# Kernel optimization log

Measured on AMD Instinct MI355X. Metric: run time of the kernel, lower is better.

Reference implementation:

```python
import math
import jax, jax.numpy as jnp
import numpy as np

BS, Q_LEN, DIM = 8, 16, 4096
MAX_SEQ = 4096
N_Q_HEADS, N_KV_HEADS, HEAD_DIM = 32, 8, 128
REP = N_Q_HEADS // N_KV_HEADS


def setup_inputs() -> dict:
    key = jax.random.key(0)
    ks = jax.random.split(key, 12)
    w = 0.02
    return {
        "x": jax.random.normal(ks[0], (BS, Q_LEN, DIM), jnp.float32),
        "k_cache": jax.random.normal(ks[1], (BS, MAX_SEQ, N_KV_HEADS, HEAD_DIM), jnp.float32),
        "v_cache": jax.random.normal(ks[2], (BS, MAX_SEQ, N_KV_HEADS, HEAD_DIM), jnp.float32),
        "Wq": jax.random.normal(ks[3], (DIM, N_Q_HEADS * HEAD_DIM), jnp.float32) * w,
        "bq": jax.random.normal(ks[4], (N_Q_HEADS * HEAD_DIM,), jnp.float32) * w,
        "Wk": jax.random.normal(ks[5], (DIM, N_KV_HEADS * HEAD_DIM), jnp.float32) * w,
        "bk": jax.random.normal(ks[6], (N_KV_HEADS * HEAD_DIM,), jnp.float32) * w,
        "Wv": jax.random.normal(ks[7], (DIM, N_KV_HEADS * HEAD_DIM), jnp.float32) * w,
        "bv": jax.random.normal(ks[8], (N_KV_HEADS * HEAD_DIM,), jnp.float32) * w,
        "Wo": jax.random.normal(ks[9], (N_Q_HEADS * HEAD_DIM, DIM), jnp.float32) * w,
        "bo": jax.random.normal(ks[10], (DIM,), jnp.float32) * w,
        "start_pos": MAX_SEQ - Q_LEN,
        "seq_len_for_kv": Q_LEN,
    }


def reference(x, k_cache, v_cache, Wq, bq, Wk, bk, Wv, bv, Wo, bo, start_pos, seq_len_for_kv):
    bs, sl, dim = x.shape
    # Projections (torch Linear: x @ W^T + b; here W stored as [in, out])
    q = (x @ Wq + bq).reshape(bs, sl, N_KV_HEADS, REP, HEAD_DIM)  # [b, q, g, r, d]
    k = (x @ Wk + bk).reshape(bs, sl, N_KV_HEADS, HEAD_DIM)
    v = (x @ Wv + bv).reshape(bs, sl, N_KV_HEADS, HEAD_DIM)
    # KV-cache append (start_pos / seq_len_for_kv are static Python ints)
    k_cache = k_cache.at[:, start_pos:start_pos + seq_len_for_kv].set(k)
    v_cache = v_cache.at[:, start_pos:start_pos + seq_len_for_kv].set(v)
    kv_len = start_pos + seq_len_for_kv
    keys = k_cache[:, :kv_len]    # [b, L, g, d]
    vals = v_cache[:, :kv_len]    # [b, L, g, d]
    # GQA: each kv head g serves REP query heads r (broadcast instead of repeat_kv)
    scale = 1.0 / math.sqrt(HEAD_DIM)
    scores = jnp.einsum('bqgrd,blgd->bgrql', q, keys) * scale  # [b, g, r, q, L]
    att = jax.nn.softmax(scores, axis=-1)
    out = jnp.einsum('bgrql,blgd->bqgrd', att, vals)           # [b, q, g, r, d]
    out = out.reshape(bs, sl, N_Q_HEADS * HEAD_DIM)
    return out @ Wo + bo
```

## Files before the change

kernel.cpp:

```cpp
#include <hip/hip_runtime.h>
#include <math.h>

#define DIM       4096
#define NKVH      8
#define HD        128
#define MAX_SEQ   4096
#define START_POS 4080
#define NQKV      6144
#define NCHUNK    8
#define CHUNK     512
#define KS        8
#define ATT_SCALE 0.08838834764831845f

#define WS_PART   0
#define WS_QH     6291456
#define WS_QL     6553600
#define WS_KNEW   6815744
#define WS_VNEW   6946816
#define WS_PM     7077888
#define WS_PL     7110656
#define WS_ATH    7143424
#define WS_ATL    7405568
#define WS_XH     7667712
#define WS_XL     7929856
#define WS_PARTO  WS_PART

typedef __bf16 bf16x8 __attribute__((ext_vector_type(8)));
typedef float  f32x4  __attribute__((ext_vector_type(4)));
typedef unsigned int uintx4 __attribute__((ext_vector_type(4)));

__device__ __forceinline__ unsigned short f2bf(float f) {
    return __builtin_bit_cast(unsigned short, (__bf16)f);
}
__device__ __forceinline__ float bf2f(unsigned short h) {
    union { unsigned int u; float f; } v; v.u = ((unsigned int)h) << 16;
    return v.f;
}
__device__ __forceinline__ void splitbf(float f, unsigned short &h, unsigned short &l) {
    h = f2bf(f);
    l = f2bf(f - bf2f(h));
}
__device__ __forceinline__ bf16x8 ldsfrag(const unsigned short* p) {
    uintx4 u = *(const uintx4*)p;
    return __builtin_bit_cast(bf16x8, u);
}
__device__ __forceinline__ bf16x8 ldsfrag2(const unsigned short* p) {
    union { uint2 u2[2]; bf16x8 v; } u;
    u.u2[0] = *(const uint2*)p;
    u.u2[1] = *(const uint2*)(p + 4);
    return u.v;
}
#define MFMA16(a,b,c) __builtin_amdgcn_mfma_f32_16x16x32_bf16(a, b, c, 0, 0, 0)
#define VCOMP(v,j) ((j)==0?(v).x:((j)==1?(v).y:((j)==2?(v).z:(v).w)))

__global__ __launch_bounds__(256) void split_x_kernel(
    const float* __restrict__ x, unsigned short* __restrict__ xh,
    unsigned short* __restrict__ xl, int n)
{
    int i = blockIdx.x * 256 + threadIdx.x;
    if (i < n) { unsigned short h, l; splitbf(x[i], h, l); xh[i] = h; xl[i] = l; }
}

__device__ __forceinline__ void gemm_body(
    const unsigned short* __restrict__ Ah, const unsigned short* __restrict__ Al,
    const float* __restrict__ W, int ldW, int noff,
    float* __restrict__ part, int partStride, int ncol0, int ks,
    unsigned short* Ahs, unsigned short* Als, unsigned short* Bs)
{
    const int t = threadIdx.x;
    const int w = t >> 6, lane = t & 63, l15 = lane & 15, quad = lane >> 4;
    f32x4 acc[2][4];
    #pragma unroll
    for (int i = 0; i < 2; ++i)
        #pragma unroll
        for (int nt = 0; nt < 4; ++nt) acc[i][nt] = (f32x4){0.f, 0.f, 0.f, 0.f};

    const int k0base = ks * 512;
    uintx4 areg_h[4], areg_l[4];
    float4 wreg[4];

    auto LOAD = [&](int it) {
        int k0 = k0base + it * 64;
        #pragma unroll
        for (int i = 0; i < 4; ++i) {
            int f = t + i * 256;
            int row = f >> 3, c0 = (f & 7) << 3;
            size_t off = (size_t)row * DIM + k0 + c0;
            areg_h[i] = *(const uintx4*)(Ah + off);
            areg_l[i] = *(const uintx4*)(Al + off);
        }
        #pragma unroll
        for (int i = 0; i < 4; ++i) {
            int kk = (t >> 4) + 16 * i;
            int n0 = (t & 15) << 2;
            wreg[i] = *(const float4*)(W + (size_t)(k0 + kk) * ldW + noff + n0);
        }
    };

    LOAD(0);
    for (int it = 0; it < 8; ++it) {
        __syncthreads();
        #pragma unroll
        for (int i = 0; i < 4; ++i) {
            int f = t + i * 256;
            int row = f >> 3, c0 = (f & 7) << 3;
            *(uintx4*)(Ahs + row * 72 + c0) = areg_h[i];
            *(uintx4*)(Als + row * 72 + c0) = areg_l[i];
        }
        {
            int n0 = (t & 15) << 2;
            #pragma unroll
            for (int i = 0; i < 4; ++i) {
                int kk = (t >> 4) + 16 * i;
                #pragma unroll
                for (int j = 0; j < 4; ++j)
                    Bs[(n0 + j) * 68 + kk] = f2bf(VCOMP(wreg[i], j));
            }
        }
        __syncthreads();
        if (it < 7) LOAD(it + 1);
        #pragma unroll
        for (int kt = 0; kt < 2; ++kt) {
            int ko = kt * 32 + quad * 8;
            bf16x8 ah0 = ldsfrag(Ahs + ((2*w+0)*16 + l15) * 72 + ko);
            bf16x8 ah1 = ldsfrag(Ahs + ((2*w+1)*16 + l15) * 72 + ko);
            bf16x8 al0 = ldsfrag(Als + ((2*w+0)*16 + l15) * 72 + ko);
            bf16x8 al1 = ldsfrag(Als + ((2*w+1)*16 + l15) * 72 + ko);
            #pragma unroll
            for (int nt = 0; nt < 4; ++nt) {
                bf16x8 b = ldsfrag2(Bs + (nt*16 + l15) * 68 + ko);
                acc[0][nt] = MFMA16(ah0, b, acc[0][nt]);
                acc[0][nt] = MFMA16(al0, b, acc[0][nt]);
                acc[1][nt] = MFMA16(ah1, b, acc[1][nt]);
                acc[1][nt] = MFMA16(al1, b, acc[1][nt]);
            }
        }
    }
    #pragma unroll
    for (int i = 0; i < 2; ++i)
        #pragma unroll
        for (int nt = 0; nt < 4; ++nt)
            #pragma unroll
            for (int r = 0; r < 4; ++r) {
                int row = (2*w + i) * 16 + quad * 4 + r;
                int col = ncol0 + nt * 16 + l15;
                part[(size_t)(ks * 128 + row) * partStride + col] = acc[i][nt][r];
            }
}

__global__ __launch_bounds__(256) void qkv_gemm_kernel(
    const unsigned short* __restrict__ xh, const unsigned short* __restrict__ xl,
    const float* __restrict__ Wq, const float* __restrict__ Wk,
    const float* __restrict__ Wv, float* __restrict__ part)
{
    __shared__ unsigned short Ahs[128 * 72], Als[128 * 72];
    __shared__ unsigned short Bs[64 * 68];
    int ncol0 = blockIdx.x * 64;
    int ks = blockIdx.y;
    const float* W; int ldW, noff;
    if (ncol0 < 4096)      { W = Wq; ldW = 4096; noff = ncol0; }
    else if (ncol0 < 5120) { W = Wk; ldW = 1024; noff = ncol0 - 4096; }
    else                   { W = Wv; ldW = 1024; noff = ncol0 - 5120; }
    gemm_body(xh, xl, W, ldW, noff, part, NQKV, ncol0, ks, Ahs, Als, Bs);
}

__global__ __launch_bounds__(256) void oproj_gemm_kernel(
    const unsigned short* __restrict__ ah, const unsigned short* __restrict__ al,
    const float* __restrict__ Wo, float* __restrict__ part)
{
    __shared__ unsigned short Ahs[128 * 72], Als[128 * 72];
    __shared__ unsigned short Bs[64 * 68];
    int ncol0 = blockIdx.x * 64;
    int ks = blockIdx.y;
    gemm_body(ah, al, Wo, 4096, ncol0, part, 4096, ncol0, ks, Ahs, Als, Bs);
}

__global__ __launch_bounds__(256) void qkv_reduce_kernel(
    const float* __restrict__ part, const float* __restrict__ bq,
    const float* __restrict__ bk, const float* __restrict__ bv,
    unsigned short* __restrict__ qh, unsigned short* __restrict__ ql,
    float* __restrict__ k_new, float* __restrict__ v_new)
{
    int gid = blockIdx.x * 256 + threadIdx.x;
    int row = gid / NQKV;
    int n   = gid - row * NQKV;
    float s = 0.f;
    #pragma unroll
    for (int j = 0; j < KS; ++j)
        s += part[(size_t)(j * 128 + row) * NQKV + n];
    if (n < 4096) {
        float v = s + bq[n];
        unsigned short h, l; splitbf(v, h, l);
        qh[row * 4096 + n] = h; ql[row * 4096 + n] = l;
    } else if (n < 5120) k_new[row * 1024 + (n - 4096)] = s + bk[n - 4096];
    else                 v_new[row * 1024 + (n - 5120)] = s + bv[n - 5120];
}

__global__ __launch_bounds__(512, 2) void attn_partial5_kernel(
    const unsigned short* __restrict__ qhp, const unsigned short* __restrict__ qlp,
    const float* __restrict__ kc, const float* __restrict__ vc,
    const float* __restrict__ knew, const float* __restrict__ vnew,
    float* __restrict__ part_O, float* __restrict__ part_m, float* __restrict__ part_l)
{
    __shared__ unsigned short Kb[2][32][136];
    __shared__ unsigned short Vt[2][128][44];
    __shared__ unsigned short Pw[8][16 * 36];

    const int t = threadIdx.x;
    const int w = t >> 6, lane = t & 63, l15 = lane & 15, quad = lane >> 4;
    const int gsel = w >> 2;
    const int rep  = w & 3;
    const int blk = blockIdx.x;
    const int b = blk >> 5, gg = (blk >> 3) & 3, c = blk & 7;
    const int g = gg * 2 + gsel;

    const int p0 = t >> 6;
    const int q4 = t & 63;
    const int gl = q4 >> 5;
    const int d0 = (q4 & 31) << 2;

    bf16x8 qhf[4], qlf[4];
    {
        size_t base = (size_t)(b * 16 + l15) * DIM + (g * 4 + rep) * HD + quad * 8;
        #pragma unroll
        for (int kt = 0; kt < 4; ++kt) {
            qhf[kt] = ldsfrag(qhp + base + kt * 32);
            qlf[kt] = ldsfrag(qlp + base + kt * 32);
        }
    }

    float m_run[4], l_run[4];
    f32x4 oacc[8];
    #pragma unroll
    for (int r = 0; r < 4; ++r) { m_run[r] = -INFINITY; l_run[r] = 0.f; }
    #pragma unroll
    for (int d = 0; d < 8; ++d) oacc[d] = (f32x4){0.f, 0.f, 0.f, 0.f};

    float4 kreg[4], vreg[4];
    auto LOADKV = [&](int it) {
        #pragma unroll
        for (int i = 0; i < 4; ++i) {
            int pos = p0 + i * 8;
            int pg = c * CHUNK + it * 32 + pos;
            const float *ksrc, *vsrc;
            if (pg >= START_POS) {
                size_t off = (size_t)(b * 16 + pg - START_POS) * (NKVH * HD) + gg * 256 + q4 * 4;
                ksrc = knew + off; vsrc = vnew + off;
            } else {
                size_t off = ((size_t)(b * MAX_SEQ + pg) * NKVH) * HD + gg * 256 + q4 * 4;
                ksrc = kc + off; vsrc = vc + off;
            }
            kreg[i] = *(const float4*)ksrc;
            vreg[i] = *(const float4*)vsrc;
        }
    };

    unsigned short* phw = Pw[w];

    LOADKV(0);
    for (int it = 0; it < 16; ++it) {
        __syncthreads();
        #pragma unroll
        for (int i = 0; i < 4; ++i) {
            int pos = p0 + i * 8;
            ushort4 k4 = make_ushort4(f2bf(kreg[i].x), f2bf(kreg[i].y),
                                      f2bf(kreg[i].z), f2bf(kreg[i].w));
            *(ushort4*)&Kb[gl][pos][d0] = k4;
        }
        #pragma unroll
        for (int j = 0; j < 4; ++j) {
            ushort4 v4 = make_ushort4(f2bf(VCOMP(vreg[0], j)), f2bf(VCOMP(vreg[1], j)),
                                      f2bf(VCOMP(vreg[2], j)), f2bf(VCOMP(vreg[3], j)));
            *(ushort4*)&Vt[gl][d0 + j][p0 * 4] = v4;
        }
        __syncthreads();
        if (it + 1 < 16) LOADKV(it + 1);

        f32x4 sacc[2];
        sacc[0] = (f32x4){0.f,0.f,0.f,0.f};
        sacc[1] = (f32x4){0.f,0.f,0.f,0.f};
        #pragma unroll
        for (int nt = 0; nt < 2; ++nt)
            #pragma unroll
            for (int kt = 0; kt < 4; ++kt) {
                bf16x8 bh = ldsfrag(&Kb[gsel][nt*16 + l15][kt*32 + quad*8]);
                sacc[nt] = MFMA16(qhf[kt], bh, sacc[nt]);
                sacc[nt] = MFMA16(qlf[kt], bh, sacc[nt]);
            }

        float e0[4], e1[4], alpha[4];
        #pragma unroll
        for (int r = 0; r < 4; ++r) {
            float s0 = sacc[0][r] * ATT_SCALE;
            float s1 = sacc[1][r] * ATT_SCALE;
            float mx = fmaxf(s0, s1);
            mx = fmaxf(mx, __shfl_xor(mx, 1));
            mx = fmaxf(mx, __shfl_xor(mx, 2));
            mx = fmaxf(mx, __shfl_xor(mx, 4));
            mx = fmaxf(mx, __shfl_xor(mx, 8));
            float mnew = fmaxf(m_run[r], mx);
            alpha[r] = __expf(m_run[r] - mnew);
            e0[r] = __expf(s0 - mnew);
            e1[r] = __expf(s1 - mnew);
            float sum = e0[r] + e1[r];
            sum += __shfl_xor(sum, 1);
            sum += __shfl_xor(sum, 2);
            sum += __shfl_xor(sum, 4);
            sum += __shfl_xor(sum, 8);
            l_run[r] = l_run[r] * alpha[r] + sum;
            m_run[r] = mnew;
        }
        #pragma unroll
        for (int d = 0; d < 8; ++d)
            #pragma unroll
            for (int r = 0; r < 4; ++r) oacc[d][r] *= alpha[r];

        {
            int slot0 = 4 * (l15 & 7) + (l15 >> 3);
            #pragma unroll
            for (int r = 0; r < 4; ++r) {
                phw[(quad*4 + r) * 36 + slot0]     = f2bf(e0[r]);
                phw[(quad*4 + r) * 36 + slot0 + 2] = f2bf(e1[r]);
            }
        }
        bf16x8 pa = ldsfrag(phw + l15 * 36 + quad * 8);

        #pragma unroll
        for (int dt = 0; dt < 8; ++dt) {
            bf16x8 vb = ldsfrag(&Vt[gsel][dt*16 + l15][quad * 8]);
            oacc[dt] = MFMA16(pa, vb, oacc[dt]);
        }
    }

    const size_t obase = (size_t)((b * 8 + g) * 8 + c) * 64 + rep * 16 + quad * 4;
    #pragma unroll
    for (int dt = 0; dt < 8; ++dt)
        #pragma unroll
        for (int r = 0; r < 4; ++r)
            part_O[(obase + r) * HD + dt * 16 + l15] = oacc[dt][r];
    if (l15 == 0) {
        #pragma unroll
        for (int r = 0; r < 4; ++r) {
            part_m[obase + r] = m_run[r];
            part_l[obase + r] = l_run[r];
        }
    }
}

__global__ __launch_bounds__(128) void attn_combine_kernel(
    const float* __restrict__ part_O, const float* __restrict__ part_m,
    const float* __restrict__ part_l, unsigned short* __restrict__ ah,
    unsigned short* __restrict__ al)
{
    int bid = blockIdx.x;
    int d = threadIdx.x;
    int bg = bid >> 6;
    int row = bid & 63;
    float mc[NCHUNK], lc[NCHUNK];
    float M = -INFINITY;
    #pragma unroll
    for (int cc = 0; cc < NCHUNK; ++cc) {
        mc[cc] = part_m[(bg * NCHUNK + cc) * 64 + row];
        lc[cc] = part_l[(bg * NCHUNK + cc) * 64 + row];
        M = fmaxf(M, mc[cc]);
    }
    float L = 0.f, acc = 0.f;
    #pragma unroll
    for (int cc = 0; cc < NCHUNK; ++cc) {
        float wgt = __expf(mc[cc] - M);
        L += lc[cc] * wgt;
        acc += part_O[((size_t)(bg * NCHUNK + cc) * 64 + row) * HD + d] * wgt;
    }
    int b = bg >> 3, g = bg & 7;
    int r = row >> 4, qp = row & 15;
    float v = acc / L;
    unsigned short h, l; splitbf(v, h, l);
    size_t idx = (size_t)(b * 16 + qp) * DIM + (g * 4 + r) * HD + d;
    ah[idx] = h; al[idx] = l;
}

__global__ __launch_bounds__(256) void oproj_reduce_kernel(
    const float* __restrict__ part, const float* __restrict__ bo,
    float* __restrict__ out)
{
    int gid = blockIdx.x * 256 + threadIdx.x;
    int n = gid & 4095;
    float s = 0.f;
    #pragma unroll
    for (int j = 0; j < KS; ++j) s += part[(size_t)j * 524288 + gid];
    out[gid] = s + bo[n];
}

extern "C" void kernel_launch(void* const* d_in, const int* in_sizes, int n_in,
                              void* d_out, int out_size, void* d_ws, size_t ws_size,
                              hipStream_t stream)
{
    const float* x  = (const float*)d_in[0];
    const float* kc = (const float*)d_in[1];
    const float* vc = (const float*)d_in[2];
    const float* Wq = (const float*)d_in[3];
    const float* bq = (const float*)d_in[4];
    const float* Wk = (const float*)d_in[5];
    const float* bk = (const float*)d_in[6];
    const float* Wv = (const float*)d_in[7];
    const float* bv = (const float*)d_in[8];
    const float* Wo = (const float*)d_in[9];
    const float* bo = (const float*)d_in[10];
    float* out = (float*)d_out;
    float* ws  = (float*)d_ws;

    unsigned short* xh = (unsigned short*)(ws + WS_XH);
    unsigned short* xl = (unsigned short*)(ws + WS_XL);
    unsigned short* qh = (unsigned short*)(ws + WS_QH);
    unsigned short* ql = (unsigned short*)(ws + WS_QL);
    unsigned short* ath = (unsigned short*)(ws + WS_ATH);
    unsigned short* atl = (unsigned short*)(ws + WS_ATL);

    split_x_kernel<<<2048, 256, 0, stream>>>(x, xh, xl, 524288);
    qkv_gemm_kernel<<<dim3(96, KS), 256, 0, stream>>>(xh, xl, Wq, Wk, Wv, ws + WS_PART);
    qkv_reduce_kernel<<<3072, 256, 0, stream>>>(ws + WS_PART, bq, bk, bv,
                                                qh, ql, ws + WS_KNEW, ws + WS_VNEW);
    attn_partial5_kernel<<<256, 512, 0, stream>>>(qh, ql, kc, vc,
                                                  ws + WS_KNEW, ws + WS_VNEW,
                                                  ws + WS_PARTO, ws + WS_PM, ws + WS_PL);
    attn_combine_kernel<<<4096, 128, 0, stream>>>(ws + WS_PARTO, ws + WS_PM,
                                                  ws + WS_PL, ath, atl);
    oproj_gemm_kernel<<<dim3(64, KS), 256, 0, stream>>>(ath, atl, Wo, ws + WS_PART);
    oproj_reduce_kernel<<<2048, 256, 0, stream>>>(ws + WS_PART, bo, out);
}
```

Before: 438.9 us.

## Double attention KV tile to 64 positions and vectorize split/reduce kernels

The attention kernel now processes 64 KV positions per iteration instead of 32, halving loop trips and barriers and issuing twice as many MFMAs and loads per sync. The P and V tiles are widened to match, with a new slot layout. The split and reduce kernels are vectorized to float4 loads and stores with a quarter of the threads. In exchange, the larger register prefetch (16 float4) and bigger LDS footprint may strain occupancy under the 512x2 launch bound.

```diff
diff --git a/kernel.cpp b/kernel.cpp
--- a/kernel.cpp
+++ b/kernel.cpp
@@ -55,10 +55,19 @@
 
 __global__ __launch_bounds__(256) void split_x_kernel(
     const float* __restrict__ x, unsigned short* __restrict__ xh,
-    unsigned short* __restrict__ xl, int n)
+    unsigned short* __restrict__ xl, int n4)
 {
     int i = blockIdx.x * 256 + threadIdx.x;
-    if (i < n) { unsigned short h, l; splitbf(x[i], h, l); xh[i] = h; xl[i] = l; }
+    if (i < n4) {
+        float4 v = *(const float4*)(x + (size_t)i * 4);
+        ushort4 h, l;
+        splitbf(v.x, h.x, l.x);
+        splitbf(v.y, h.y, l.y);
+        splitbf(v.z, h.z, l.z);
+        splitbf(v.w, h.w, l.w);
+        *(ushort4*)(xh + (size_t)i * 4) = h;
+        *(ushort4*)(xl + (size_t)i * 4) = l;
+    }
 }
 
 __device__ __forceinline__ void gemm_body(
@@ -182,29 +191,44 @@
     float* __restrict__ k_new, float* __restrict__ v_new)
 {
     int gid = blockIdx.x * 256 + threadIdx.x;
-    int row = gid / NQKV;
-    int n   = gid - row * NQKV;
-    float s = 0.f;
-    #pragma unroll
-    for (int j = 0; j < KS; ++j)
-        s += part[(size_t)(j * 128 + row) * NQKV + n];
+    int row = gid / 1536;
+    int c4  = gid - row * 1536;
+    int n = c4 * 4;
+    float4 s = make_float4(0.f, 0.f, 0.f, 0.f);
+    #pragma unroll
+    for (int j = 0; j < KS; ++j) {
+        float4 p = *(const float4*)&part[(size_t)(j * 128 + row) * NQKV + n];
+        s.x += p.x; s.y += p.y; s.z += p.z; s.w += p.w;
+    }
     if (n < 4096) {
-        float v = s + bq[n];
-        unsigned short h, l; splitbf(v, h, l);
-        qh[row * 4096 + n] = h; ql[row * 4096 + n] = l;
-    } else if (n < 5120) k_new[row * 1024 + (n - 4096)] = s + bk[n - 4096];
-    else                 v_new[row * 1024 + (n - 5120)] = s + bv[n - 5120];
-}
-
-__global__ __launch_bounds__(512, 2) void attn_partial5_kernel(
+        float4 b4 = *(const float4*)&bq[n];
+        ushort4 h, l;
+        splitbf(s.x + b4.x, h.x, l.x);
+        splitbf(s.y + b4.y, h.y, l.y);
+        splitbf(s.z + b4.z, h.z, l.z);
+        splitbf(s.w + b4.w, h.w, l.w);
+        *(ushort4*)&qh[row * 4096 + n] = h;
+        *(ushort4*)&ql[row * 4096 + n] = l;
+    } else if (n < 5120) {
+        float4 b4 = *(const float4*)&bk[n - 4096];
+        float4 o = make_float4(s.x + b4.x, s.y + b4.y, s.z + b4.z, s.w + b4.w);
+        *(float4*)&k_new[row * 1024 + (n - 4096)] = o;
+    } else {
+        float4 b4 = *(const float4*)&bv[n - 5120];
+        float4 o = make_float4(s.x + b4.x, s.y + b4.y, s.z + b4.z, s.w + b4.w);
+        *(float4*)&v_new[row * 1024 + (n - 5120)] = o;
+    }
+}
+
+__global__ __launch_bounds__(512, 2) void attn_partial7_kernel(
     const unsigned short* __restrict__ qhp, const unsigned short* __restrict__ qlp,
     const float* __restrict__ kc, const float* __restrict__ vc,
     const float* __restrict__ knew, const float* __restrict__ vnew,
     float* __restrict__ part_O, float* __restrict__ part_m, float* __restrict__ part_l)
 {
-    __shared__ unsigned short Kb[2][32][136];
-    __shared__ unsigned short Vt[2][128][44];
-    __shared__ unsigned short Pw[8][16 * 36];
+    __shared__ unsigned short Kb[2][64][136];
+    __shared__ unsigned short Vt[2][128][76];
+    __shared__ unsigned short Pw[8][16 * 76];
 
     const int t = threadIdx.x;
     const int w = t >> 6, lane = t & 63, l15 = lane & 15, quad = lane >> 4;
@@ -236,12 +260,12 @@
     #pragma unroll
     for (int d = 0; d < 8; ++d) oacc[d] = (f32x4){0.f, 0.f, 0.f, 0.f};
 
-    float4 kreg[4], vreg[4];
+    float4 kreg[8], vreg[8];
     auto LOADKV = [&](int it) {
         #pragma unroll
-        for (int i = 0; i < 4; ++i) {
+        for (int i = 0; i < 8; ++i) {
             int pos = p0 + i * 8;
-            int pg = c * CHUNK + it * 32 + pos;
+            int pg = c * CHUNK + it * 64 + pos;
             const float *ksrc, *vsrc;
             if (pg >= START_POS) {
                 size_t off = (size_t)(b * 16 + pg - START_POS) * (NKVH * HD) + gg * 256 + q4 * 4;
@@ -256,12 +280,13 @@
     };
 
     unsigned short* phw = Pw[w];
+    const int slotbase = (l15 & 7) * 8 + (l15 >> 3);
 
     LOADKV(0);
-    for (int it = 0; it < 16; ++it) {
+    for (int it = 0; it < 8; ++it) {
         __syncthreads();
         #pragma unroll
-        for (int i = 0; i < 4; ++i) {
+        for (int i = 0; i < 8; ++i) {
             int pos = p0 + i * 8;
             ushort4 k4 = make_ushort4(f2bf(kreg[i].x), f2bf(kreg[i].y),
                                       f2bf(kreg[i].z), f2bf(kreg[i].w));
@@ -269,18 +294,21 @@
         }
         #pragma unroll
         for (int j = 0; j < 4; ++j) {
-            ushort4 v4 = make_ushort4(f2bf(VCOMP(vreg[0], j)), f2bf(VCOMP(vreg[1], j)),
-                                      f2bf(VCOMP(vreg[2], j)), f2bf(VCOMP(vreg[3], j)));
-            *(ushort4*)&Vt[gl][d0 + j][p0 * 4] = v4;
+            ushort4 vlo = make_ushort4(f2bf(VCOMP(vreg[0], j)), f2bf(VCOMP(vreg[1], j)),
+                                       f2bf(VCOMP(vreg[2], j)), f2bf(VCOMP(vreg[3], j)));
+            ushort4 vhi = make_ushort4(f2bf(VCOMP(vreg[4], j)), f2bf(VCOMP(vreg[5], j)),
+                                       f2bf(VCOMP(vreg[6], j)), f2bf(VCOMP(vreg[7], j)));
+            *(ushort4*)&Vt[gl][d0 + j][p0 * 8]     = vlo;
+            *(ushort4*)&Vt[gl][d0 + j][p0 * 8 + 4] = vhi;
         }
         __syncthreads();
-        if (it + 1 < 16) LOADKV(it + 1);
-
-        f32x4 sacc[2];
-        sacc[0] = (f32x4){0.f,0.f,0.f,0.f};
-        sacc[1] = (f32x4){0.f,0.f,0.f,0.f};
-        #pragma unroll
-        for (int nt = 0; nt < 2; ++nt)
+        if (it + 1 < 8) LOADKV(it + 1);
+
+        f32x4 sacc[4];
+        #pragma unroll
+        for (int nt = 0; nt < 4; ++nt) sacc[nt] = (f32x4){0.f,0.f,0.f,0.f};
+        #pragma unroll
+        for (int nt = 0; nt < 4; ++nt)
             #pragma unroll
             for (int kt = 0; kt < 4; ++kt) {
                 bf16x8 bh = ldsfrag(&Kb[gsel][nt*16 + l15][kt*32 + quad*8]);
@@ -288,12 +316,14 @@
                 sacc[nt] = MFMA16(qlf[kt], bh, sacc[nt]);
             }
 
-        float e0[4], e1[4], alpha[4];
+        float e0[4], e1[4], e2[4], e3[4], alpha[4];
         #pragma unroll
         for (int r = 0; r < 4; ++r) {
             float s0 = sacc[0][r] * ATT_SCALE;
             float s1 = sacc[1][r] * ATT_SCALE;
-            float mx = fmaxf(s0, s1);
+            float s2 = sacc[2][r] * ATT_SCALE;
+            float s3 = sacc[3][r] * ATT_SCALE;
+            float mx = fmaxf(fmaxf(s0, s1), fmaxf(s2, s3));
             mx = fmaxf(mx, __shfl_xor(mx, 1));
             mx = fmaxf(mx, __shfl_xor(mx, 2));
             mx = fmaxf(mx, __shfl_xor(mx, 4));
@@ -302,7 +332,9 @@
             alpha[r] = __expf(m_run[r] - mnew);
             e0[r] = __expf(s0 - mnew);
             e1[r] = __expf(s1 - mnew);
-            float sum = e0[r] + e1[r];
+            e2[r] = __expf(s2 - mnew);
+            e3[r] = __expf(s3 - mnew);
+            float sum = (e0[r] + e1[r]) + (e2[r] + e3[r]);
             sum += __shfl_xor(sum, 1);
             sum += __shfl_xor(sum, 2);
             sum += __shfl_xor(sum, 4);
@@ -315,20 +347,23 @@
             #pragma unroll
             for (int r = 0; r < 4; ++r) oacc[d][r] *= alpha[r];
 
-        {
-            int slot0 = 4 * (l15 & 7) + (l15 >> 3);
-            #pragma unroll
-            for (int r = 0; r < 4; ++r) {
-                phw[(quad*4 + r) * 36 + slot0]     = f2bf(e0[r]);
-                phw[(quad*4 + r) * 36 + slot0 + 2] = f2bf(e1[r]);
-            }
-        }
-        bf16x8 pa = ldsfrag(phw + l15 * 36 + quad * 8);
+        #pragma unroll
+        for (int r = 0; r < 4; ++r) {
+            unsigned short* pr = phw + (quad*4 + r) * 76 + slotbase;
+            pr[0] = f2bf(e0[r]);
+            pr[2] = f2bf(e1[r]);
+            pr[4] = f2bf(e2[r]);
+            pr[6] = f2bf(e3[r]);
+        }
+        bf16x8 pa0 = ldsfrag2(phw + l15 * 76 + quad * 8);
+        bf16x8 pa1 = ldsfrag2(phw + l15 * 76 + 32 + quad * 8);
 
         #pragma unroll
         for (int dt = 0; dt < 8; ++dt) {
-            bf16x8 vb = ldsfrag(&Vt[gsel][dt*16 + l15][quad * 8]);
-            oacc[dt] = MFMA16(pa, vb, oacc[dt]);
+            bf16x8 vb0 = ldsfrag2(&Vt[gsel][dt*16 + l15][quad * 8]);
+            oacc[dt] = MFMA16(pa0, vb0, oacc[dt]);
+            bf16x8 vb1 = ldsfrag2(&Vt[gsel][dt*16 + l15][32 + quad * 8]);
+            oacc[dt] = MFMA16(pa1, vb1, oacc[dt]);
         }
     }
 
@@ -383,12 +418,17 @@
     const float* __restrict__ part, const float* __restrict__ bo,
     float* __restrict__ out)
 {
-    int gid = blockIdx.x * 256 + threadIdx.x;
-    int n = gid & 4095;
-    float s = 0.f;
-    #pragma unroll
-    for (int j = 0; j < KS; ++j) s += part[(size_t)j * 524288 + gid];
-    out[gid] = s + bo[n];
+    int gid4 = blockIdx.x * 256 + threadIdx.x;
+    int n = (gid4 & 1023) * 4;
+    float4 s = make_float4(0.f, 0.f, 0.f, 0.f);
+    #pragma unroll
+    for (int j = 0; j < KS; ++j) {
+        float4 p = *(const float4*)&part[(size_t)j * 524288 + (size_t)gid4 * 4];
+        s.x += p.x; s.y += p.y; s.z += p.z; s.w += p.w;
+    }
+    float4 b4 = *(const float4*)&bo[n];
+    float4 o = make_float4(s.x + b4.x, s.y + b4.y, s.z + b4.z, s.w + b4.w);
+    *(float4*)&out[(size_t)gid4 * 4] = o;
 }
 
 extern "C" void kernel_launch(void* const* d_in, const int* in_sizes, int n_in,
@@ -416,15 +456,15 @@
     unsigned short* ath = (unsigned short*)(ws + WS_ATH);
     unsigned short* atl = (unsigned short*)(ws + WS_ATL);
 
-    split_x_kernel<<<2048, 256, 0, stream>>>(x, xh, xl, 524288);
+    split_x_kernel<<<512, 256, 0, stream>>>(x, xh, xl, 131072);
     qkv_gemm_kernel<<<dim3(96, KS), 256, 0, stream>>>(xh, xl, Wq, Wk, Wv, ws + WS_PART);
-    qkv_reduce_kernel<<<3072, 256, 0, stream>>>(ws + WS_PART, bq, bk, bv,
-                                                qh, ql, ws + WS_KNEW, ws + WS_VNEW);
-    attn_partial5_kernel<<<256, 512, 0, stream>>>(qh, ql, kc, vc,
+    qkv_reduce_kernel<<<768, 256, 0, stream>>>(ws + WS_PART, bq, bk, bv,
+                                               qh, ql, ws + WS_KNEW, ws + WS_VNEW);
+    attn_partial7_kernel<<<256, 512, 0, stream>>>(qh, ql, kc, vc,
                                                   ws + WS_KNEW, ws + WS_VNEW,
                                                   ws + WS_PARTO, ws + WS_PM, ws + WS_PL);
     attn_combine_kernel<<<4096, 128, 0, stream>>>(ws + WS_PARTO, ws + WS_PM,
                                                   ws + WS_PL, ath, atl);
     oproj_gemm_kernel<<<dim3(64, KS), 256, 0, stream>>>(ath, atl, Wo, ws + WS_PART);
-    oproj_reduce_kernel<<<2048, 256, 0, stream>>>(ws + WS_PART, bo, out);
-}
+    oproj_reduce_kernel<<<512, 256, 0, stream>>>(ws + WS_PART, bo, out);
+}
```

Result: no change. 435.8 us (-0.7%).
